# Performance work log

Measured on AMD Instinct MI355X. Metric: run time of the kernel, lower is better.

The kernel has to match this reference:

```python
import jax, jax.numpy as jnp
import numpy as np

N_DOMAINS = 4          # number of unique domain labels in d
NUM_PROJ = 50          # hard-coded in DiscriminativeSlicedWasserstein.__init__
P_POW = 2              # hard-coded p=2


def setup_inputs() -> dict:
    key = jax.random.key(0)
    k1, k2, k3 = jax.random.split(key, 3)
    N, IN_DIM, OUT_DIM = 32768, 2048, 512
    z = jax.random.normal(k1, (N, IN_DIM), dtype=jnp.float32)
    W = jax.random.normal(k2, (IN_DIM, OUT_DIM), dtype=jnp.float32) * 0.02
    b = jnp.zeros((OUT_DIM,), dtype=jnp.float32)
    # random projections on the unit sphere (rows normalized), as in rand_projections
    P = jax.random.normal(k3, (NUM_PROJ, OUT_DIM), dtype=jnp.float32)
    P = P / jnp.sqrt(jnp.sum(P * P, axis=1, keepdims=True))
    # sorted, equal-count domain labels -> grouping becomes a static reshape
    d = jnp.repeat(jnp.arange(N_DOMAINS, dtype=jnp.int32), N // N_DOMAINS)
    return {"z": z, "W": W, "b": b, "P": P, "d": d}


def reference(z, W, b, P, d):
    # z = self.D(z): linear discriminator
    h = z @ W + b                                   # [N, out_dim]
    per = h.shape[0] // N_DOMAINS
    groups = h.reshape(N_DOMAINS, per, -1)          # [G, n, out_dim] (d is sorted equal-count)
    # project each group onto the random directions: z.matmul(P.T)
    proj = jnp.einsum('gnd,kd->gnk', groups, P)     # [G, n, num_proj]
    # sort along the sample axis (torch sorts each projection's values)
    srt = jnp.sort(proj, axis=1)                    # [G, n, num_proj]
    # all domain pairs (itertools.combinations); equal group sizes => mean of
    # per-pair means == mean over the stacked pair differences
    ii, jj = np.triu_indices(N_DOMAINS, k=1)
    diff = srt[jj] - srt[ii]                        # [n_pairs, n, num_proj]
    loss = jnp.mean(diff ** P_POW)
    return loss
```

## Files before the change

### kernel.cpp

```cpp
#include <hip/hip_runtime.h>

#define NROWS 32768
#define KDIM  2048
#define DDIM  512
#define NPROJ 50
#define NDOM  4
#define NPER  8192
#define BNPAD 64
#define PELEM ((size_t)NDOM * NPROJ * NPER)

typedef __attribute__((ext_vector_type(8))) short short8v;
typedef __attribute__((ext_vector_type(4))) float f32x4;

__device__ inline ushort bf16_rne(float x) {
  union { float f; unsigned u; } v; v.f = x;
  unsigned r = v.u + 0x7FFF + ((v.u >> 16) & 1);
  return (ushort)(r >> 16);
}
__device__ inline float bf16_f32(ushort h) {
  union { unsigned u; float f; } v; v.u = ((unsigned)h) << 16;
  return v.f;
}

__global__ __launch_bounds__(256) void wp_kernel(const float* __restrict__ W,
                                                 const float* __restrict__ b,
                                                 const float* __restrict__ P,
                                                 ushort* __restrict__ Bpk,
                                                 float* __restrict__ bp) {
  int idx = blockIdx.x * 256 + threadIdx.x;
  if (idx >= (KDIM + 1) * BNPAD) return;
  int i = idx >> 6;
  int c = idx & 63;
  float acc = 0.f;
  if (c < NPROJ) {
    const float4* row = (const float4*)((i < KDIM) ? (W + (size_t)i * DDIM) : b);
    const float4* pr  = (const float4*)(P + (size_t)c * DDIM);
#pragma unroll 4
    for (int d = 0; d < DDIM / 4; ++d) {
      float4 w = row[d], p = pr[d];
      acc += w.x * p.x + w.y * p.y + w.z * p.z + w.w * p.w;
    }
  }
  if (i < KDIM) {
    int tg = i >> 5, kb = (i >> 3) & 3, e = i & 7;
    int m = c & 15, cf = c >> 4;
    size_t pos = (size_t)(tg * 4 + cf) * 1024 + (kb * 16 + m) * 8 + e;
    ushort h = bf16_rne(acc);
    Bpk[pos]       = h;
    Bpk[pos + 512] = bf16_rne(acc - bf16_f32(h));
  } else {
    bp[c] = acc;
  }
}

__device__ __forceinline__ void split8_trunc(const float4 f0, const float4 f1,
                                             short8v& hi, short8v& lo) {
  const float a[8] = {f0.x, f0.y, f0.z, f0.w, f1.x, f1.y, f1.z, f1.w};
  union { unsigned u[4]; short8v s; } H, L;
#pragma unroll
  for (int p = 0; p < 4; ++p) {
    float a0 = a[2 * p], a1 = a[2 * p + 1];
    unsigned u0 = __float_as_uint(a0), u1 = __float_as_uint(a1);
    H.u[p] = __builtin_amdgcn_perm(u1, u0, 0x07060302);
    float l0 = a0 - __uint_as_float(u0 & 0xFFFF0000u);
    float l1 = a1 - __uint_as_float(u1 & 0xFFFF0000u);
    L.u[p] = __builtin_amdgcn_perm(__float_as_uint(l1), __float_as_uint(l0), 0x07060302);
  }
  hi = H.s; lo = L.s;
}

__device__ __forceinline__ void gload16(const float* g, float* l) {
  __builtin_amdgcn_global_load_lds(
      (const __attribute__((address_space(1))) unsigned int*)(unsigned long long)g,
      (__attribute__((address_space(3))) unsigned int*)(unsigned int)(unsigned long long)l,
      16, 0, 0);
}

__global__ __launch_bounds__(256) void gemm_mfma(const float* __restrict__ z,
                                                 const ushort* __restrict__ Bpk,
                                                 const float* __restrict__ bp,
                                                 float* __restrict__ part) {
  __shared__ __align__(16) float A_lds[2][4096];
  __shared__ __align__(16) float B_lds[2][2048];

  const int tid  = threadIdx.x;
  const int lane = tid & 63;
  const int wave = tid >> 6;
  const int m    = lane & 15;
  const int kb   = lane >> 4;
  const int row0 = blockIdx.x * 128;
  const int ksb  = blockIdx.y;
  const int k0   = ksb * 1024;

  const float* gsrcA[4];
  const float* gsrcB[2];
  const float* Bf = (const float*)Bpk;
#pragma unroll
  for (int a = 0; a < 4; ++a) {
    const int i = wave * 4 + a;
    const int r = i * 8 + (lane >> 3);
    const int q = (lane & 7) ^ ((lane >> 3) & 7);
    gsrcA[a] = z + (size_t)(row0 + r) * KDIM + k0 + q * 4;
  }
#pragma unroll
  for (int b2 = 0; b2 < 2; ++b2) {
    const int j = wave * 2 + b2;
    gsrcB[b2] = Bf + (size_t)(k0 >> 5) * 2048 + j * 256 + lane * 4;
  }

#define STAGE(buf_, t_)                                                   \
  {                                                                       \
    _Pragma("unroll")                                                     \
    for (int a = 0; a < 4; ++a)                                           \
      gload16(gsrcA[a] + (t_) * 32, &A_lds[buf_][(wave * 4 + a) * 256]);  \
    _Pragma("unroll")                                                     \
    for (int b2 = 0; b2 < 2; ++b2)                                        \
      gload16(gsrcB[b2] + (size_t)(t_) * 2048,                            \
              &B_lds[buf_][(wave * 2 + b2) * 256]);                       \
  }

  f32x4 acc[2][4];
#pragma unroll
  for (int rf = 0; rf < 2; ++rf)
#pragma unroll
    for (int cf = 0; cf < 4; ++cf) acc[rf][cf] = (f32x4)0.f;

  STAGE(0, 0);

#pragma unroll 2
  for (int t = 0; t < 32; ++t) {
    const int buf = t & 1;

    if (t < 31) {
      STAGE(buf ^ 1, t + 1);
      asm volatile("s_waitcnt vmcnt(6)" ::: "memory");
    } else {
      asm volatile("s_waitcnt vmcnt(0)" ::: "memory");
    }
    __builtin_amdgcn_s_barrier();
    __builtin_amdgcn_sched_barrier(0);

    float4 f[2][2];
#pragma unroll
    for (int rf = 0; rf < 2; ++rf) {
      const int r = wave * 32 + rf * 16 + m;
      const float* base = &A_lds[buf][r * 32];
      f[rf][0] = *(const float4*)(base + (((kb * 2)     ^ (m & 7)) * 4));
      f[rf][1] = *(const float4*)(base + (((kb * 2 + 1) ^ (m & 7)) * 4));
    }
    short8v bh[4], bl[4];
    const ushort* Bu = (const ushort*)&B_lds[buf][0];
#pragma unroll
    for (int cf = 0; cf < 4; ++cf) {
      const ushort* fb = Bu + cf * 1024 + lane * 8;
      bh[cf] = *(const short8v*)fb;
      bl[cf] = *(const short8v*)(fb + 512);
    }

    short8v ah[2], al[2];
#pragma unroll
    for (int rf = 0; rf < 2; ++rf)
      split8_trunc(f[rf][0], f[rf][1], ah[rf], al[rf]);

#pragma unroll
    for (int cf = 0; cf < 4; ++cf)
#pragma unroll
      for (int rf = 0; rf < 2; ++rf) {
        acc[rf][cf] = __builtin_amdgcn_mfma_f32_16x16x32_bf16(ah[rf], bh[cf], acc[rf][cf], 0, 0, 0);
        acc[rf][cf] = __builtin_amdgcn_mfma_f32_16x16x32_bf16(al[rf], bh[cf], acc[rf][cf], 0, 0, 0);
        acc[rf][cf] = __builtin_amdgcn_mfma_f32_16x16x32_bf16(ah[rf], bl[cf], acc[rf][cf], 0, 0, 0);
      }

    __builtin_amdgcn_s_barrier();
  }
#undef STAGE

  const int g = row0 >> 13;
#pragma unroll
  for (int rf = 0; rf < 2; ++rf) {
    const int nbase = (row0 & (NPER - 1)) + wave * 32 + rf * 16 + kb * 4;
#pragma unroll
    for (int cf = 0; cf < 4; ++cf) {
      const int col = cf * 16 + m;
      if (col < NPROJ) {
        const float bj = (ksb == 0) ? bp[col] : 0.f;
        float* dst = part + (size_t)ksb * PELEM +
                     (size_t)(g * NPROJ + col) * NPER + nbase;
        dst[0] = acc[rf][cf][0] + bj;
        dst[1] = acc[rf][cf][1] + bj;
        dst[2] = acc[rf][cf][2] + bj;
        dst[3] = acc[rf][cf][3] + bj;
      }
    }
  }
}

#define CE(a, b, asc) { float x_ = v[a], y_ = v[b]; \
  if ((asc) ? (x_ > y_) : (x_ < y_)) { v[a] = y_; v[b] = x_; } }

__device__ inline int swz(int i) { return i ^ (((i >> 5) & 7) << 2); }
#define SPAD 8192

template <int JMAX>
__device__ inline void wave_merge(float v[8], int t, int k) {
  const bool asc = (((t << 3) & k) == 0);
#pragma unroll
  for (int j = JMAX; j >= 8; j >>= 1) {
    const int d = j >> 3;
    const bool keepmin = (asc != ((t & d) != 0));
#pragma unroll
    for (int e = 0; e < 8; ++e) {
      float o = __shfl_xor(v[e], d, 64);
      v[e] = keepmin ? fminf(v[e], o) : fmaxf(v[e], o);
    }
  }
  CE(0, 4, asc); CE(1, 5, asc); CE(2, 6, asc); CE(3, 7, asc);
  CE(0, 2, asc); CE(1, 3, asc); CE(4, 6, asc); CE(5, 7, asc);
  CE(0, 1, asc); CE(2, 3, asc); CE(4, 5, asc); CE(6, 7, asc);
}

__global__ __launch_bounds__(1024) void sort_cols(float* __restrict__ p0,
                                                  const float* __restrict__ p1) {
  __shared__ __align__(16) float sA[SPAD];
  __shared__ __align__(16) float sB[SPAD];
  float* col = p0 + (size_t)blockIdx.x * NPER;
  const int t  = threadIdx.x;
  const int i0 = t << 3;
  float v[8];

  *(float4*)&v[0] = *(const float4*)(col + i0);
  *(float4*)&v[4] = *(const float4*)(col + i0 + 4);
  {
    const float* c1 = p1 + (size_t)blockIdx.x * NPER;
    float4 a0 = *(const float4*)(c1 + i0), a1 = *(const float4*)(c1 + i0 + 4);
    v[0] += a0.x; v[1] += a0.y; v[2] += a0.z; v[3] += a0.w;
    v[4] += a1.x; v[5] += a1.y; v[6] += a1.z; v[7] += a1.w;
  }

  CE(0, 1, true);  CE(2, 3, false); CE(4, 5, true);  CE(6, 7, false);
  CE(0, 2, true);  CE(1, 3, true);  CE(4, 6, false); CE(5, 7, false);
  CE(0, 1, true);  CE(2, 3, true);  CE(4, 5, false); CE(6, 7, false);
  {
    bool d8 = (t & 1) == 0;
    CE(0, 4, d8); CE(1, 5, d8); CE(2, 6, d8); CE(3, 7, d8);
    CE(0, 2, d8); CE(1, 3, d8); CE(4, 6, d8); CE(5, 7, d8);
    CE(0, 1, d8); CE(2, 3, d8); CE(4, 5, d8); CE(6, 7, d8);
  }

  wave_merge<8>(v, t, 16);
  wave_merge<16>(v, t, 32);
  wave_merge<32>(v, t, 64);
  wave_merge<64>(v, t, 128);
  wave_merge<128>(v, t, 256);
  wave_merge<256>(v, t, 512);

  *(float4*)&sA[swz(i0)]     = *(float4*)&v[0];
  *(float4*)&sA[swz(i0 + 4)] = *(float4*)&v[4];
  __syncthreads();
  int cur = 0;

  for (int k = 1024; k <= NPER; k <<= 1) {
    const bool asc = ((i0 & k) == 0);
    for (int j = k >> 1; j >= 512; j >>= 1) {
      const float* src = cur ? sB : sA;
      float*       dst = cur ? sA : sB;
      const int ip = i0 ^ j;
      float4 a0 = *(const float4*)&src[swz(i0)];
      float4 a1 = *(const float4*)&src[swz(i0 + 4)];
      float4 b0 = *(const float4*)&src[swz(ip)];
      float4 b1 = *(const float4*)&src[swz(ip + 4)];
      const bool keepmin = (asc != ((i0 & j) != 0));
      float4 r0, r1;
      if (keepmin) {
        r0.x = fminf(a0.x, b0.x); r0.y = fminf(a0.y, b0.y); r0.z = fminf(a0.z, b0.z); r0.w = fminf(a0.w, b0.w);
        r1.x = fminf(a1.x, b1.x); r1.y = fminf(a1.y, b1.y); r1.z = fminf(a1.z, b1.z); r1.w = fminf(a1.w, b1.w);
      } else {
        r0.x = fmaxf(a0.x, b0.x); r0.y = fmaxf(a0.y, b0.y); r0.z = fmaxf(a0.z, b0.z); r0.w = fmaxf(a0.w, b0.w);
        r1.x = fmaxf(a1.x, b1.x); r1.y = fmaxf(a1.y, b1.y); r1.z = fmaxf(a1.z, b1.z); r1.w = fmaxf(a1.w, b1.w);
      }
      *(float4*)&dst[swz(i0)]     = r0;
      *(float4*)&dst[swz(i0 + 4)] = r1;
      __syncthreads();
      cur ^= 1;
      *(float4*)&v[0] = r0;
      *(float4*)&v[4] = r1;
    }
    wave_merge<256>(v, t, k);
    if (k != NPER) {
      float* d2 = cur ? sB : sA;
      *(float4*)&d2[swz(i0)]     = *(float4*)&v[0];
      *(float4*)&d2[swz(i0 + 4)] = *(float4*)&v[4];
      __syncthreads();
    }
  }

  *(float4*)(col + i0)     = *(float4*)&v[0];
  *(float4*)(col + i0 + 4) = *(float4*)&v[4];
}

__global__ __launch_bounds__(256) void reduce_k(const float* __restrict__ projT,
                                                float* __restrict__ partial) {
  const int k  = blockIdx.x;
  const int nc = blockIdx.y;
  const int n  = nc * 1024 + threadIdx.x * 4;
  const float4 x0 = *(const float4*)(projT + (size_t)(0 * NPROJ + k) * NPER + n);
  const float4 x1 = *(const float4*)(projT + (size_t)(1 * NPROJ + k) * NPER + n);
  const float4 x2 = *(const float4*)(projT + (size_t)(2 * NPROJ + k) * NPER + n);
  const float4 x3 = *(const float4*)(projT + (size_t)(3 * NPROJ + k) * NPER + n);
  const float a0[4] = {x0.x, x0.y, x0.z, x0.w};
  const float a1[4] = {x1.x, x1.y, x1.z, x1.w};
  const float a2[4] = {x2.x, x2.y, x2.z, x2.w};
  const float a3[4] = {x3.x, x3.y, x3.z, x3.w};
  float local = 0.f;
#pragma unroll
  for (int e = 0; e < 4; ++e) {
    float d01 = a0[e] - a1[e], d02 = a0[e] - a2[e], d03 = a0[e] - a3[e];
    float d12 = a1[e] - a2[e], d13 = a1[e] - a3[e], d23 = a2[e] - a3[e];
    local += d01 * d01 + d02 * d02 + d03 * d03 + d12 * d12 + d13 * d13 + d23 * d23;
  }
#pragma unroll
  for (int o = 32; o > 0; o >>= 1) local += __shfl_down(local, o, 64);
  __shared__ float red[4];
  if ((threadIdx.x & 63) == 0) red[threadIdx.x >> 6] = local;
  __syncthreads();
  if (threadIdx.x == 0) partial[nc * NPROJ + k] = red[0] + red[1] + red[2] + red[3];
}

__global__ __launch_bounds__(512) void final_k(const float* __restrict__ partial,
                                               float* __restrict__ out) {
  const int t = threadIdx.x;
  float v = (t < 8 * NPROJ) ? partial[t] : 0.f;
#pragma unroll
  for (int o = 32; o > 0; o >>= 1) v += __shfl_down(v, o, 64);
  __shared__ float red[8];
  if ((t & 63) == 0) red[t >> 6] = v;
  __syncthreads();
  if (t == 0) {
    float s = 0.f;
#pragma unroll
    for (int w = 0; w < 8; ++w) s += red[w];
    out[0] = s * (1.0f / (6.0f * NPER * NPROJ));
  }
}

extern "C" void kernel_launch(void* const* d_in, const int* in_sizes, int n_in,
                              void* d_out, int out_size, void* d_ws, size_t ws_size,
                              hipStream_t stream) {
  const float* z = (const float*)d_in[0];
  const float* W = (const float*)d_in[1];
  const float* b = (const float*)d_in[2];
  const float* P = (const float*)d_in[3];

  float*  part0   = (float*)d_ws;
  float*  part1   = part0 + PELEM;
  ushort* Bpk     = (ushort*)(part1 + PELEM);
  float*  bp      = (float*)(Bpk + (size_t)2 * BNPAD * KDIM);
  float*  partial = bp + BNPAD;

  wp_kernel<<<((KDIM + 1) * BNPAD + 255) / 256, 256, 0, stream>>>(W, b, P, Bpk, bp);
  gemm_mfma<<<dim3(NROWS / 128, 2), 256, 0, stream>>>(z, Bpk, bp, part0);
  sort_cols<<<NDOM * NPROJ, 1024, 0, stream>>>(part0, part1);
  reduce_k<<<dim3(NPROJ, 8), 256, 0, stream>>>(part0, partial);
  final_k<<<1, 512, 0, stream>>>(partial, (float*)d_out);
}
```

Baseline: 129.4 us.

## Use 256-row 512-thread GEMM tiles with 4-way split-K and reordered prefetch

The GEMM block grows to 8 waves covering 256 rows, and K is split four ways instead of two, giving 128x4 blocks. Each block's B tile is now shared by twice as many rows. The next-stage global->LDS prefetch is issued after the LDS fragment reads, with a __syncthreads at the end of each step, replacing the manual vmcnt waits. The sort kernel now sums four split-K partial buffers, which adds workspace and extra global reads in exchange for more GEMM parallelism and B reuse.

```diff
diff --git a/kernel.cpp b/kernel.cpp
--- a/kernel.cpp
+++ b/kernel.cpp
@@ -76,11 +76,13 @@
       16, 0, 0);
 }
 
-__global__ __launch_bounds__(256) void gemm_mfma(const float* __restrict__ z,
+__global__ __launch_bounds__(512) void gemm_mfma(const float* __restrict__ z,
                                                  const ushort* __restrict__ Bpk,
                                                  const float* __restrict__ bp,
                                                  float* __restrict__ part) {
-  __shared__ __align__(16) float A_lds[2][4096];
+  constexpr int KSLICE = KDIM / 4;
+  constexpr int NSTEP  = KSLICE / 32;
+  __shared__ __align__(16) float A_lds[2][256 * 32];
   __shared__ __align__(16) float B_lds[2][2048];
 
   const int tid  = threadIdx.x;
@@ -88,35 +90,26 @@
   const int wave = tid >> 6;
   const int m    = lane & 15;
   const int kb   = lane >> 4;
-  const int row0 = blockIdx.x * 128;
+  const int row0 = blockIdx.x * 256;
   const int ksb  = blockIdx.y;
-  const int k0   = ksb * 1024;
+  const int k0   = ksb * KSLICE;
 
   const float* gsrcA[4];
-  const float* gsrcB[2];
   const float* Bf = (const float*)Bpk;
 #pragma unroll
   for (int a = 0; a < 4; ++a) {
-    const int i = wave * 4 + a;
-    const int r = i * 8 + (lane >> 3);
+    const int r = wave * 32 + a * 8 + (lane >> 3);
     const int q = (lane & 7) ^ ((lane >> 3) & 7);
     gsrcA[a] = z + (size_t)(row0 + r) * KDIM + k0 + q * 4;
   }
-#pragma unroll
-  for (int b2 = 0; b2 < 2; ++b2) {
-    const int j = wave * 2 + b2;
-    gsrcB[b2] = Bf + (size_t)(k0 >> 5) * 2048 + j * 256 + lane * 4;
-  }
-
-#define STAGE(buf_, t_)                                                   \
-  {                                                                       \
-    _Pragma("unroll")                                                     \
-    for (int a = 0; a < 4; ++a)                                           \
-      gload16(gsrcA[a] + (t_) * 32, &A_lds[buf_][(wave * 4 + a) * 256]);  \
-    _Pragma("unroll")                                                     \
-    for (int b2 = 0; b2 < 2; ++b2)                                        \
-      gload16(gsrcB[b2] + (size_t)(t_) * 2048,                            \
-              &B_lds[buf_][(wave * 2 + b2) * 256]);                       \
+  const float* gsrcB = Bf + (size_t)(k0 >> 5) * 2048 + wave * 256 + lane * 4;
+
+#define STAGE(buf_, t_)                                                      \
+  {                                                                          \
+    _Pragma("unroll")                                                        \
+    for (int a = 0; a < 4; ++a)                                              \
+      gload16(gsrcA[a] + (t_) * 32, &A_lds[buf_][(wave * 32 + a * 8) * 32]); \
+    gload16(gsrcB + (size_t)(t_) * 2048, &B_lds[buf_][wave * 256]);          \
   }
 
   f32x4 acc[2][4];
@@ -126,19 +119,11 @@
     for (int cf = 0; cf < 4; ++cf) acc[rf][cf] = (f32x4)0.f;
 
   STAGE(0, 0);
+  __syncthreads();
 
 #pragma unroll 2
-  for (int t = 0; t < 32; ++t) {
+  for (int t = 0; t < NSTEP; ++t) {
     const int buf = t & 1;
-
-    if (t < 31) {
-      STAGE(buf ^ 1, t + 1);
-      asm volatile("s_waitcnt vmcnt(6)" ::: "memory");
-    } else {
-      asm volatile("s_waitcnt vmcnt(0)" ::: "memory");
-    }
-    __builtin_amdgcn_s_barrier();
-    __builtin_amdgcn_sched_barrier(0);
 
     float4 f[2][2];
 #pragma unroll
@@ -156,6 +141,10 @@
       bh[cf] = *(const short8v*)fb;
       bl[cf] = *(const short8v*)(fb + 512);
     }
+    __builtin_amdgcn_sched_barrier(0);
+
+    if (t < NSTEP - 1) STAGE(buf ^ 1, t + 1);
+    __builtin_amdgcn_sched_barrier(0);
 
     short8v ah[2], al[2];
 #pragma unroll
@@ -171,7 +160,7 @@
         acc[rf][cf] = __builtin_amdgcn_mfma_f32_16x16x32_bf16(ah[rf], bl[cf], acc[rf][cf], 0, 0, 0);
       }
 
-    __builtin_amdgcn_s_barrier();
+    __syncthreads();
   }
 #undef STAGE
 
@@ -220,7 +209,9 @@
 }
 
 __global__ __launch_bounds__(1024) void sort_cols(float* __restrict__ p0,
-                                                  const float* __restrict__ p1) {
+                                                  const float* __restrict__ p1,
+                                                  const float* __restrict__ p2,
+                                                  const float* __restrict__ p3) {
   __shared__ __align__(16) float sA[SPAD];
   __shared__ __align__(16) float sB[SPAD];
   float* col = p0 + (size_t)blockIdx.x * NPER;
@@ -232,9 +223,15 @@
   *(float4*)&v[4] = *(const float4*)(col + i0 + 4);
   {
     const float* c1 = p1 + (size_t)blockIdx.x * NPER;
+    const float* c2 = p2 + (size_t)blockIdx.x * NPER;
+    const float* c3 = p3 + (size_t)blockIdx.x * NPER;
     float4 a0 = *(const float4*)(c1 + i0), a1 = *(const float4*)(c1 + i0 + 4);
-    v[0] += a0.x; v[1] += a0.y; v[2] += a0.z; v[3] += a0.w;
-    v[4] += a1.x; v[5] += a1.y; v[6] += a1.z; v[7] += a1.w;
+    float4 b0 = *(const float4*)(c2 + i0), b1 = *(const float4*)(c2 + i0 + 4);
+    float4 d0 = *(const float4*)(c3 + i0), d1 = *(const float4*)(c3 + i0 + 4);
+    v[0] += a0.x + b0.x + d0.x; v[1] += a0.y + b0.y + d0.y;
+    v[2] += a0.z + b0.z + d0.z; v[3] += a0.w + b0.w + d0.w;
+    v[4] += a1.x + b1.x + d1.x; v[5] += a1.y + b1.y + d1.y;
+    v[6] += a1.z + b1.z + d1.z; v[7] += a1.w + b1.w + d1.w;
   }
 
   CE(0, 1, true);  CE(2, 3, false); CE(4, 5, true);  CE(6, 7, false);
@@ -353,13 +350,15 @@
 
   float*  part0   = (float*)d_ws;
   float*  part1   = part0 + PELEM;
-  ushort* Bpk     = (ushort*)(part1 + PELEM);
+  float*  part2   = part1 + PELEM;
+  float*  part3   = part2 + PELEM;
+  ushort* Bpk     = (ushort*)(part3 + PELEM);
   float*  bp      = (float*)(Bpk + (size_t)2 * BNPAD * KDIM);
   float*  partial = bp + BNPAD;
 
   wp_kernel<<<((KDIM + 1) * BNPAD + 255) / 256, 256, 0, stream>>>(W, b, P, Bpk, bp);
-  gemm_mfma<<<dim3(NROWS / 128, 2), 256, 0, stream>>>(z, Bpk, bp, part0);
-  sort_cols<<<NDOM * NPROJ, 1024, 0, stream>>>(part0, part1);
+  gemm_mfma<<<dim3(NROWS / 256, 4), 512, 0, stream>>>(z, Bpk, bp, part0);
+  sort_cols<<<NDOM * NPROJ, 1024, 0, stream>>>(part0, part1, part2, part3);
   reduce_k<<<dim3(NPROJ, 8), 256, 0, stream>>>(part0, partial);
   final_k<<<1, 512, 0, stream>>>(partial, (float*)d_out);
 }
```

Measured after the change: 140.7 us. +8.8%, slower.
